# Kernel tuning notes

Measured on AMD Instinct MI355X. Metric: run time of the kernel, lower is better.

## Reference

```python
import jax, jax.numpy as jnp
import numpy as np

P0 = 2   # tublet_size
P = 16   # patch_size
FC = 2   # flow channels (map_x, map_y)


def patchify(x, p0, p1, p2):
    # x: (B, C, T, H, W) -> (B, (T/p0)(H/p1)(W/p2), p0*p1*p2*C)
    B, C, T, H, W = x.shape
    x = x.reshape(B, C, T // p0, p0, H // p1, p1, W // p2, p2)
    x = x.transpose(0, 2, 4, 6, 3, 5, 7, 1)  # b t h w p0 p1 p2 c
    return x.reshape(B, (T // p0) * (H // p1) * (W // p2), p0 * p1 * p2 * C)


def unpatchify(x, p0, p1, p2, C, T, H, W):
    # x: (B, N, p0*p1*p2*C) -> (B, C, T, H, W)
    B = x.shape[0]
    x = x.reshape(B, T // p0, H // p1, W // p2, p0, p1, p2, C)
    x = x.transpose(0, 7, 1, 4, 2, 5, 3, 6)  # b c t p0 h p1 w p2
    return x.reshape(B, C, T, H, W)


def bilinear_warp(imgs, mx, my):
    # imgs: (B, C, T, H, W); mx, my: (B, T, H, W) absolute sample coords.
    # Equivalent of cv2.remap INTER_LINEAR with constant (zero) border.
    B, C, T, H, W = imgs.shape
    x0 = jnp.floor(mx)
    y0 = jnp.floor(my)
    wx = (mx - x0).reshape(B, 1, T, H * W)
    wy = (my - y0).reshape(B, 1, T, H * W)
    x0i = x0.astype(jnp.int32)
    y0i = y0.astype(jnp.int32)
    imgs_flat = imgs.reshape(B, C, T, H * W)

    def gather(yi, xi):
        yc = jnp.clip(yi, 0, H - 1)
        xc = jnp.clip(xi, 0, W - 1)
        idx = (yc * W + xc).reshape(B, 1, T, H * W)
        v = jnp.take_along_axis(imgs_flat, jnp.broadcast_to(idx, (B, C, T, H * W)), axis=-1)
        valid = ((yi >= 0) & (yi <= H - 1) & (xi >= 0) & (xi <= W - 1)).reshape(B, 1, T, H * W)
        return v * valid.astype(v.dtype)

    v00 = gather(y0i, x0i)
    v01 = gather(y0i, x0i + 1)
    v10 = gather(y0i + 1, x0i)
    v11 = gather(y0i + 1, x0i + 1)
    out = (v00 * (1 - wx) * (1 - wy) + v01 * wx * (1 - wy)
           + v10 * (1 - wx) * wy + v11 * wx * wy)
    return out.reshape(B, C, T, H, W)


def setup_inputs() -> dict:
    key = jax.random.key(0)
    k1, k2, k3 = jax.random.split(key, 3)
    B, C, T, H, W = 8, 3, 16, 224, 224
    N = (T // P0) * (H // P) * (W // P)         # 1568 tokens
    D = P0 * P * P * FC                         # 1024 per-token flow dim
    output = jax.random.normal(k1, (B, N, D), dtype=jnp.float32)
    raw_target = jax.random.normal(k2, (B, C, T, H, W), dtype=jnp.float32)
    mask = jax.random.randint(k3, (B, N), 0, 2) > 0
    return {"output": output, "raw_target": raw_target, "mask": mask}


def reference(output, raw_target, mask):
    B, C, T, H, W = raw_target.shape
    # tokens -> dense flow field (B, 2, T, H, W)
    flows = unpatchify(output, P0, P, P, FC, T, H, W)
    gx = jnp.arange(W, dtype=flows.dtype)               # (W,)
    gy = jnp.arange(H, dtype=flows.dtype)[:, None]      # (H, 1)
    mx = flows[:, 0] + gx                                # (B, T, H, W)
    my = flows[:, 1] + gy
    recons = bilinear_warp(raw_target, mx, my)           # (B, C, T, H, W)
    rec_p = patchify(recons, P0, P, P)                   # (B, N, p0*p1*p2*C)
    tgt_p = patchify(raw_target, P0, P, P)
    m = mask.astype(rec_p.dtype)[..., None]              # (B, N, 1)
    diff2 = (rec_p - tgt_p) ** 2 * m
    denom = jnp.maximum(m.sum(), 1.0) * rec_p.shape[-1]
    return diff2.sum() / denom
```

## Files before the change

kernel.cpp:

```cpp
#include <hip/hip_runtime.h>

#define Bd 8
#define Cd 3
#define Td 16
#define Hd 224
#define Wd 224
#define Nd 1568
#define Dd 1024
#define HWd (Hd*Wd)
#define MASK_N (Bd*Nd)
#define PATCH_ELEMS 1536.0

#define WIN 32
#define PITCH 40
#define PLANE (WIN*PITCH)

__global__ void flow_mse_tok(const float* __restrict__ outp,
                             const float* __restrict__ raw,
                             const int* __restrict__ mask,
                             float* __restrict__ partial) {
    const int tk = blockIdx.x;
    const int tid = threadIdx.x;

    if (mask[tk] == 0) {
        if (tid == 0) partial[tk] = 0.f;
        return;
    }

    const int b = tk / Nd;
    const int n = tk - b * Nd;
    const int t2  = n / 196;
    const int rem = n - t2 * 196;
    const int ph  = rem / 14;
    const int pw  = rem - ph * 14;

    const int WX = min(max(pw * 16 - 8, 0), Wd - WIN);
    const int WY = min(max(ph * 16 - 8, 0), Hd - WIN);

    __shared__ float lds[6 * PLANE];

    {
        const int r  = tid >> 4;
        const int cc = (tid & 15) << 1;
        #pragma unroll
        for (int p = 0; p < 6; ++p) {
            const int c  = p >> 1;
            const int i0 = p & 1;
            const int t  = (t2 << 1) + i0;
            const float* img = raw + (size_t)(((b * Cd + c) * Td + t)) * HWd;
            float2 a = *(const float2*)(img + (WY + r)      * Wd + WX + cc);
            float2 d = *(const float2*)(img + (WY + r + 16) * Wd + WX + cc);
            float* pl = lds + p * PLANE;
            pl[r * PITCH + cc]            = a.x;
            pl[r * PITCH + cc + 1]        = a.y;
            pl[(r + 16) * PITCH + cc]     = d.x;
            pl[(r + 16) * PITCH + cc + 1] = d.y;
        }
    }
    __syncthreads();

    const int i1 = tid >> 4;
    const int i2 = tid & 15;
    const int h = (ph << 4) + i1;
    const int w = (pw << 4) + i2;
    const int tIdx = (h - WY) * PITCH + (w - WX);

    const float* fptr = outp + (size_t)tk * Dd;

    float acc = 0.f;
    #pragma unroll
    for (int i0 = 0; i0 < 2; ++i0) {
        const int t = (t2 << 1) + i0;
        float2 f = *(const float2*)(fptr + (((i0 << 8) + tid) << 1));
        float mx = f.x + (float)w;
        float my = f.y + (float)h;

        float x0 = floorf(mx), y0 = floorf(my);
        float wx = mx - x0,    wy = my - y0;
        int x0i = (int)x0, y0i = (int)y0;
        int x1i = x0i + 1, y1i = y0i + 1;

        bool vx0 = (x0i >= 0) && (x0i < Wd);
        bool vx1 = (x1i >= 0) && (x1i < Wd);
        bool vy0 = (y0i >= 0) && (y0i < Hd);
        bool vy1 = (y1i >= 0) && (y1i < Hd);

        int xc0 = min(max(x0i, 0), Wd - 1);
        int xc1 = min(max(x1i, 0), Wd - 1);
        int yc0 = min(max(y0i, 0), Hd - 1);
        int yc1 = min(max(y1i, 0), Hd - 1);

        float w00 = (1.f - wx) * (1.f - wy) * ((vx0 && vy0) ? 1.f : 0.f);
        float w01 = wx         * (1.f - wy) * ((vx1 && vy0) ? 1.f : 0.f);
        float w10 = (1.f - wx) * wy         * ((vx0 && vy1) ? 1.f : 0.f);
        float w11 = wx         * wy         * ((vx1 && vy1) ? 1.f : 0.f);

        const int lx0 = xc0 - WX, lx1 = xc1 - WX;
        const int ly0 = yc0 - WY, ly1 = yc1 - WY;
        const bool ok = (lx0 >= 0) & (lx1 < WIN) & (ly0 >= 0) & (ly1 < WIN);

        if (ok) {
            const int b00 = ly0 * PITCH + lx0;
            const int b01 = ly0 * PITCH + lx1;
            const int b10 = ly1 * PITCH + lx0;
            const int b11 = ly1 * PITCH + lx1;
            #pragma unroll
            for (int c = 0; c < Cd; ++c) {
                const float* pl = lds + ((c << 1) | i0) * PLANE;
                float rec = pl[b00] * w00 + pl[b01] * w01
                          + pl[b10] * w10 + pl[b11] * w11;
                float d = rec - pl[tIdx];
                acc += d * d;
            }
        } else {
            const int i00 = yc0 * Wd + xc0;
            const int i01 = yc0 * Wd + xc1;
            const int i10 = yc1 * Wd + xc0;
            const int i11 = yc1 * Wd + xc1;
            #pragma unroll
            for (int c = 0; c < Cd; ++c) {
                const float* img = raw + (size_t)(((b * Cd + c) * Td + t)) * HWd;
                float rec = img[i00] * w00 + img[i01] * w01
                          + img[i10] * w10 + img[i11] * w11;
                const float* pl = lds + ((c << 1) | i0) * PLANE;
                float d = rec - pl[tIdx];
                acc += d * d;
            }
        }
    }

    for (int off = 32; off > 0; off >>= 1) acc += __shfl_down(acc, off, 64);
    __shared__ float sdata[4];
    int lane = tid & 63, wid = tid >> 6;
    if (lane == 0) sdata[wid] = acc;
    __syncthreads();
    if (tid == 0)
        partial[tk] = sdata[0] + sdata[1] + sdata[2] + sdata[3];
}

__global__ void finalize_kernel(const float* __restrict__ partial,
                                const int* __restrict__ mask,
                                float* __restrict__ out) {
    double s = 0.0;
    int cnt = 0;
    for (int i = threadIdx.x; i < MASK_N; i += blockDim.x) {
        s   += (double)partial[i];
        cnt += (mask[i] != 0) ? 1 : 0;
    }
    for (int off = 32; off > 0; off >>= 1) {
        s   += __shfl_down(s, off, 64);
        cnt += __shfl_down(cnt, off, 64);
    }
    __shared__ double sdat[4];
    __shared__ int    cdat[4];
    int lane = threadIdx.x & 63, wid = threadIdx.x >> 6;
    if (lane == 0) { sdat[wid] = s; cdat[wid] = cnt; }
    __syncthreads();
    if (threadIdx.x == 0) {
        double st = sdat[0] + sdat[1] + sdat[2] + sdat[3];
        int ct = cdat[0] + cdat[1] + cdat[2] + cdat[3];
        double denom = (double)(ct > 0 ? ct : 1) * PATCH_ELEMS;
        out[0] = (float)(st / denom);
    }
}

extern "C" void kernel_launch(void* const* d_in, const int* in_sizes, int n_in,
                              void* d_out, int out_size, void* d_ws, size_t ws_size,
                              hipStream_t stream) {
    const float* outp = (const float*)d_in[0];
    const float* raw  = (const float*)d_in[1];
    const int*   mask = (const int*)d_in[2];
    float* out = (float*)d_out;

    float* partial = (float*)d_ws;

    flow_mse_tok<<<MASK_N, 256, 0, stream>>>(outp, raw, mask, partial);
    finalize_kernel<<<1, 256, 0, stream>>>(partial, mask, out);
}
```

Measured before the change: 171.3 us.

## Compact masked tokens and use persistent double-buffered LDS staging kernel

Replaces the one-block-per-token launch with a compaction pass that lists the unmasked tokens, then runs a persistent grid of 1024 blocks that walks that list. Each block double-buffers the LDS window, loading the next token's image window and flow values while computing the current one, so global latency overlaps with compute. The window shrinks from 32x32 to 24x24 with a tighter margin, which cuts staging traffic but sends more samples to the slow global-memory fallback when flow displacements are large. It adds a memset and an extra kernel launch, and the grid size is fixed, so load balance depends on how many tokens are unmasked.

```diff
diff --git a/kernel.cpp b/kernel.cpp
--- a/kernel.cpp
+++ b/kernel.cpp
@@ -11,67 +11,69 @@
 #define MASK_N (Bd*Nd)
 #define PATCH_ELEMS 1536.0
 
-#define WIN 32
-#define PITCH 40
+#define WIN 24
+#define PITCH 24
 #define PLANE (WIN*PITCH)
-
-__global__ void flow_mse_tok(const float* __restrict__ outp,
-                             const float* __restrict__ raw,
-                             const int* __restrict__ mask,
-                             float* __restrict__ partial) {
-    const int tk = blockIdx.x;
-    const int tid = threadIdx.x;
-
-    if (mask[tk] == 0) {
-        if (tid == 0) partial[tk] = 0.f;
-        return;
-    }
-
-    const int b = tk / Nd;
-    const int n = tk - b * Nd;
-    const int t2  = n / 196;
-    const int rem = n - t2 * 196;
-    const int ph  = rem / 14;
-    const int pw  = rem - ph * 14;
-
-    const int WX = min(max(pw * 16 - 8, 0), Wd - WIN);
-    const int WY = min(max(ph * 16 - 8, 0), Hd - WIN);
-
-    __shared__ float lds[6 * PLANE];
-
-    {
-        const int r  = tid >> 4;
-        const int cc = (tid & 15) << 1;
-        #pragma unroll
-        for (int p = 0; p < 6; ++p) {
-            const int c  = p >> 1;
-            const int i0 = p & 1;
-            const int t  = (t2 << 1) + i0;
-            const float* img = raw + (size_t)(((b * Cd + c) * Td + t)) * HWd;
-            float2 a = *(const float2*)(img + (WY + r)      * Wd + WX + cc);
-            float2 d = *(const float2*)(img + (WY + r + 16) * Wd + WX + cc);
-            float* pl = lds + p * PLANE;
-            pl[r * PITCH + cc]            = a.x;
-            pl[r * PITCH + cc + 1]        = a.y;
-            pl[(r + 16) * PITCH + cc]     = d.x;
-            pl[(r + 16) * PITCH + cc + 1] = d.y;
+#define BUF (6*PLANE)
+#define GRID_MAIN 1024
+#define STG_V4 864
+
+struct TokGeo { int b, t2, ph, pw, WX, WY; };
+
+__device__ __forceinline__ TokGeo geo(int tk) {
+    TokGeo g;
+    g.b = tk / Nd;
+    int n = tk - g.b * Nd;
+    g.t2 = n / 196;
+    int rem = n - g.t2 * 196;
+    g.ph = rem / 14;
+    g.pw = rem - g.ph * 14;
+    g.WX = min(max(g.pw * 16 - 4, 0), Wd - WIN);
+    g.WY = min(max(g.ph * 16 - 4, 0), Hd - WIN);
+    return g;
+}
+
+__device__ __forceinline__ void stage_issue(const float* __restrict__ raw,
+                                            const TokGeo& g, int tid,
+                                            float4* st, int* loff) {
+    const float* base = raw + ((size_t)g.b * 48 + (size_t)g.t2 * 2) * HWd;
+    #pragma unroll
+    for (int k = 0; k < 4; ++k) {
+        int j = tid + k * 256;
+        if (j < STG_V4) {
+            int p   = j / 144;
+            int rem = j - p * 144;
+            int r   = rem / 6;
+            int c4  = (rem - r * 6) << 2;
+            const float* src = base + (p >> 1) * (16 * HWd) + (p & 1) * HWd
+                             + (g.WY + r) * Wd + g.WX + c4;
+            st[k] = *(const float4*)src;
+            loff[k] = p * PLANE + r * PITCH + c4;
+        } else {
+            loff[k] = -1;
         }
     }
-    __syncthreads();
-
-    const int i1 = tid >> 4;
-    const int i2 = tid & 15;
-    const int h = (ph << 4) + i1;
-    const int w = (pw << 4) + i2;
-    const int tIdx = (h - WY) * PITCH + (w - WX);
-
-    const float* fptr = outp + (size_t)tk * Dd;
-
+}
+
+__device__ __forceinline__ void stage_commit(float* __restrict__ dst,
+                                             const float4* st, const int* loff) {
+    #pragma unroll
+    for (int k = 0; k < 4; ++k)
+        if (loff[k] >= 0) *(float4*)(dst + loff[k]) = st[k];
+}
+
+__device__ __forceinline__ float compute_tok(const float* __restrict__ raw,
+                                             const float* __restrict__ pl0,
+                                             const TokGeo& g, int tid,
+                                             float2 f0, float2 f1) {
+    const int i1 = tid >> 4, i2 = tid & 15;
+    const int h = (g.ph << 4) + i1;
+    const int w = (g.pw << 4) + i2;
+    const int tIdx = (h - g.WY) * PITCH + (w - g.WX);
     float acc = 0.f;
     #pragma unroll
     for (int i0 = 0; i0 < 2; ++i0) {
-        const int t = (t2 << 1) + i0;
-        float2 f = *(const float2*)(fptr + (((i0 << 8) + tid) << 1));
+        float2 f = i0 ? f1 : f0;
         float mx = f.x + (float)w;
         float my = f.y + (float)h;
 
@@ -95,8 +97,8 @@
         float w10 = (1.f - wx) * wy         * ((vx0 && vy1) ? 1.f : 0.f);
         float w11 = wx         * wy         * ((vx1 && vy1) ? 1.f : 0.f);
 
-        const int lx0 = xc0 - WX, lx1 = xc1 - WX;
-        const int ly0 = yc0 - WY, ly1 = yc1 - WY;
+        const int lx0 = xc0 - g.WX, lx1 = xc1 - g.WX;
+        const int ly0 = yc0 - g.WY, ly1 = yc1 - g.WY;
         const bool ok = (lx0 >= 0) & (lx1 < WIN) & (ly0 >= 0) & (ly1 < WIN);
 
         if (ok) {
@@ -106,7 +108,7 @@
             const int b11 = ly1 * PITCH + lx1;
             #pragma unroll
             for (int c = 0; c < Cd; ++c) {
-                const float* pl = lds + ((c << 1) | i0) * PLANE;
+                const float* pl = pl0 + ((c << 1) | i0) * PLANE;
                 float rec = pl[b00] * w00 + pl[b01] * w01
                           + pl[b10] * w10 + pl[b11] * w11;
                 float d = rec - pl[tIdx];
@@ -117,36 +119,106 @@
             const int i01 = yc0 * Wd + xc1;
             const int i10 = yc1 * Wd + xc0;
             const int i11 = yc1 * Wd + xc1;
+            const float* base = raw + ((size_t)g.b * 48 + (size_t)g.t2 * 2 + i0) * HWd;
             #pragma unroll
             for (int c = 0; c < Cd; ++c) {
-                const float* img = raw + (size_t)(((b * Cd + c) * Td + t)) * HWd;
+                const float* img = base + c * (16 * HWd);
                 float rec = img[i00] * w00 + img[i01] * w01
                           + img[i10] * w10 + img[i11] * w11;
-                const float* pl = lds + ((c << 1) | i0) * PLANE;
+                const float* pl = pl0 + ((c << 1) | i0) * PLANE;
                 float d = rec - pl[tIdx];
                 acc += d * d;
             }
         }
     }
+    return acc;
+}
+
+__global__ void compact_kernel(const int* __restrict__ mask,
+                               int* __restrict__ list,
+                               unsigned int* __restrict__ cnt) {
+    int i = blockIdx.x * 256 + threadIdx.x;
+    bool m = (i < MASK_N) && (mask[i] != 0);
+    unsigned long long bal = __ballot(m);
+    int lane = threadIdx.x & 63;
+    int wid  = threadIdx.x >> 6;
+    unsigned pre  = (unsigned)__popcll(bal & ((1ull << lane) - 1ull));
+    unsigned wtot = (unsigned)__popcll(bal);
+    __shared__ unsigned wt[4];
+    __shared__ unsigned bbase;
+    if (lane == 0) wt[wid] = wtot;
+    __syncthreads();
+    if (threadIdx.x == 0)
+        bbase = atomicAdd(cnt, wt[0] + wt[1] + wt[2] + wt[3]);
+    __syncthreads();
+    unsigned base = bbase;
+    for (int k = 0; k < wid; ++k) base += wt[k];
+    if (m) list[base + pre] = i;
+}
+
+__global__ __launch_bounds__(256, 4)
+void flow_mse_main(const float* __restrict__ outp,
+                   const float* __restrict__ raw,
+                   const int* __restrict__ list,
+                   const unsigned int* __restrict__ cntp,
+                   float* __restrict__ partial) {
+    __shared__ float lds[2 * BUF];
+    __shared__ float sdata[4];
+    const int tid = threadIdx.x;
+    const int cnt = (int)*cntp;
+
+    float4 st[4];
+    int    loff[4];
+    float2 fc0, fc1, fn0, fn1;
+    TokGeo gc, gn;
+    float acc = 0.f;
+
+    int idx = blockIdx.x;
+    int cur = 0;
+
+    if (idx < cnt) {
+        int tk = list[idx];
+        gc = geo(tk);
+        stage_issue(raw, gc, tid, st, loff);
+        const float2* fp = (const float2*)(outp + (size_t)tk * Dd);
+        fc0 = fp[tid]; fc1 = fp[256 + tid];
+        stage_commit(lds, st, loff);
+    }
+
+    while (idx < cnt) {
+        int nidx = idx + GRID_MAIN;
+        __syncthreads();
+        bool have_next = nidx < cnt;
+        if (have_next) {
+            int ntk = list[nidx];
+            gn = geo(ntk);
+            stage_issue(raw, gn, tid, st, loff);
+            const float2* fp = (const float2*)(outp + (size_t)ntk * Dd);
+            fn0 = fp[tid]; fn1 = fp[256 + tid];
+        }
+        acc += compute_tok(raw, lds + cur * BUF, gc, tid, fc0, fc1);
+        if (have_next)
+            stage_commit(lds + (cur ^ 1) * BUF, st, loff);
+        idx = nidx; cur ^= 1;
+        gc = gn; fc0 = fn0; fc1 = fn1;
+    }
 
     for (int off = 32; off > 0; off >>= 1) acc += __shfl_down(acc, off, 64);
-    __shared__ float sdata[4];
-    int lane = tid & 63, wid = tid >> 6;
-    if (lane == 0) sdata[wid] = acc;
+    if ((tid & 63) == 0) sdata[tid >> 6] = acc;
     __syncthreads();
     if (tid == 0)
-        partial[tk] = sdata[0] + sdata[1] + sdata[2] + sdata[3];
+        partial[blockIdx.x] = sdata[0] + sdata[1] + sdata[2] + sdata[3];
 }
 
 __global__ void finalize_kernel(const float* __restrict__ partial,
                                 const int* __restrict__ mask,
                                 float* __restrict__ out) {
     double s = 0.0;
+    for (int i = threadIdx.x; i < GRID_MAIN; i += blockDim.x)
+        s += (double)partial[i];
     int cnt = 0;
-    for (int i = threadIdx.x; i < MASK_N; i += blockDim.x) {
-        s   += (double)partial[i];
+    for (int i = threadIdx.x; i < MASK_N; i += blockDim.x)
         cnt += (mask[i] != 0) ? 1 : 0;
-    }
     for (int off = 32; off > 0; off >>= 1) {
         s   += __shfl_down(s, off, 64);
         cnt += __shfl_down(cnt, off, 64);
@@ -172,8 +244,13 @@
     const int*   mask = (const int*)d_in[2];
     float* out = (float*)d_out;
 
-    float* partial = (float*)d_ws;
-
-    flow_mse_tok<<<MASK_N, 256, 0, stream>>>(outp, raw, mask, partial);
+    unsigned int* cnt = (unsigned int*)d_ws;
+    float* partial = (float*)((char*)d_ws + 16);
+    int*   list    = (int*)((char*)d_ws + 16 + GRID_MAIN * 4);
+
+    hipMemsetAsync(d_ws, 0, 16, stream);
+
+    compact_kernel<<<(MASK_N + 255) / 256, 256, 0, stream>>>(mask, list, cnt);
+    flow_mse_main<<<GRID_MAIN, 256, 0, stream>>>(outp, raw, list, cnt, partial);
     finalize_kernel<<<1, 256, 0, stream>>>(partial, mask, out);
 }
```

Result: slower. 201.2 us (+17.4%).
